# Kernel tuning notes

Hardware: AMD Instinct MI355X
Metric: run time of the kernel (lower is better)

The kernel has to match this reference:

```python
import jax, jax.numpy as jnp
import numpy as np

DIM = 1280
HEADS = 16
HD = DIM // HEADS  # 80
NSEG = 8
LSEG = 1024
SEQ = NSEG * LSEG  # 8192


def _rotate_half(x):
    x1, x2 = jnp.split(x, 2, axis=-1)
    return jnp.concatenate([-x2, x1], axis=-1)


def setup_inputs() -> dict:
    key = jax.random.key(0)
    ks = jax.random.split(key, 6)
    hidden_states = jax.random.normal(ks[0], (SEQ, DIM), dtype=jnp.float32)
    # rotary embedding table: per-position angles over head_dim
    inv_freq = 1.0 / (10000.0 ** (np.arange(0, HD, 2, dtype=np.float32) / HD))
    pos = np.arange(SEQ, dtype=np.float32)
    freqs = np.outer(pos, inv_freq)                    # [SEQ, HD/2]
    emb = np.concatenate([freqs, freqs], axis=-1)      # [SEQ, HD]
    cos = jnp.asarray(np.cos(emb), dtype=jnp.float32)
    sin = jnp.asarray(np.sin(emb), dtype=jnp.float32)
    w_scale = 1.0 / np.sqrt(DIM)
    qkv_w = jax.random.normal(ks[1], (DIM, 3 * DIM), dtype=jnp.float32) * w_scale
    qkv_b = jax.random.normal(ks[2], (3 * DIM,), dtype=jnp.float32) * 0.02
    proj_w = jax.random.normal(ks[3], (DIM, DIM), dtype=jnp.float32) * w_scale
    proj_b = jax.random.normal(ks[4], (DIM,), dtype=jnp.float32) * 0.02
    cu_seqlens = jnp.arange(NSEG + 1, dtype=jnp.int32) * LSEG
    return {
        "hidden_states": hidden_states,
        "cos": cos,
        "sin": sin,
        "qkv_w": qkv_w,
        "qkv_b": qkv_b,
        "proj_w": proj_w,
        "proj_b": proj_b,
        "cu_seqlens": cu_seqlens,
    }


def reference(hidden_states, cos, sin, qkv_w, qkv_b, proj_w, proj_b, cu_seqlens):
    S, D = hidden_states.shape
    n_seg = cu_seqlens.shape[0] - 1          # static
    L = S // n_seg                            # equal-length packed segments
    # fused QKV projection: [S, 3D] -> q, k, v each [S, H, hd]
    qkv = hidden_states @ qkv_w + qkv_b
    q, k, v = (t.reshape(S, HEADS, HD) for t in jnp.split(qkv, 3, axis=-1))
    # RoPE (computed in fp32, as in apply_rotary_pos_emb_vision)
    c = cos.astype(jnp.float32)[:, None, :]   # [S, 1, hd]
    s = sin.astype(jnp.float32)[:, None, :]
    qf = q.astype(jnp.float32)
    kf = k.astype(jnp.float32)
    q = (qf * c + _rotate_half(qf) * s).astype(q.dtype)
    k = (kf * c + _rotate_half(kf) * s).astype(k.dtype)
    # block-diagonal varlen attention == independent attention per segment
    qs = q.reshape(n_seg, L, HEADS, HD)
    ks = k.reshape(n_seg, L, HEADS, HD)
    vs = v.reshape(n_seg, L, HEADS, HD)
    scale = HD ** -0.5
    scores = jnp.einsum("nqhd,nkhd->nhqk", qs, ks) * scale
    probs = jax.nn.softmax(scores.astype(jnp.float32), axis=-1).astype(qs.dtype)
    out = jnp.einsum("nhqk,nkhd->nqhd", probs, vs)     # [n, L, H, hd]
    out = out.reshape(S, D)
    return out @ proj_w + proj_b
```

## Files before the change

### kernel.cpp

```cpp
#include <hip/hip_runtime.h>

#define SEQ   8192
#define DIM   1280
#define HEADS 16
#define HD    80
#define LSEG  1024
#define QKVD  3840

typedef unsigned short USHORT;
typedef __attribute__((ext_vector_type(8))) short bf16x8;
typedef __attribute__((ext_vector_type(4))) float f32x4;
typedef __attribute__((ext_vector_type(4))) USHORT u16x4;
typedef __attribute__((ext_vector_type(2))) unsigned uint2v;

#define CSF  0.16129832f
#define DTHR 71.554175f

__device__ __forceinline__ USHORT f2bf(float x) {
  unsigned u = __float_as_uint(x);
  u += 0x7fffu + ((u >> 16) & 1u);
  return (USHORT)(u >> 16);
}
__device__ __forceinline__ float bf2f(USHORT b) {
  return __uint_as_float(((unsigned)b) << 16);
}
__device__ __forceinline__ void gload16(const void* g, void* l) {
  __builtin_amdgcn_global_load_lds(
      (const __attribute__((address_space(1))) void*)g,
      (__attribute__((address_space(3))) void*)l, 16, 0, 0);
}
__device__ __forceinline__ unsigned cvtpk(float a, float b) {
  unsigned d;
  asm("v_cvt_pk_bf16_f32 %0, %1, %2" : "=v"(d) : "v"(a), "v"(b));
  return d;
}

__global__ __launch_bounds__(256) void conv_f2b(const float* __restrict__ in,
                                                USHORT* __restrict__ out, int n4) {
  int i = blockIdx.x * 256 + threadIdx.x;
  if (i >= n4) return;
  float4 v = reinterpret_cast<const float4*>(in)[i];
  USHORT* o = out + (size_t)i * 4;
  o[0] = f2bf(v.x); o[1] = f2bf(v.y); o[2] = f2bf(v.z); o[3] = f2bf(v.w);
}

__global__ __launch_bounds__(256) void conv_transpose(const float* __restrict__ W,
                                                      USHORT* __restrict__ Th,
                                                      int K, int N) {
  __shared__ float t[32][33];
  const int n0 = blockIdx.x * 32, k0 = blockIdx.y * 32;
  const int c = threadIdx.x & 31, r0 = threadIdx.x >> 5;
  for (int r = r0; r < 32; r += 8) t[r][c] = W[(size_t)(k0 + r) * N + n0 + c];
  __syncthreads();
  for (int r = r0; r < 32; r += 8)
    Th[(size_t)(n0 + r) * K + k0 + c] = f2bf(t[c][r]);
}

__global__ __launch_bounds__(256) void vtrans(const USHORT* __restrict__ qkv,
                                              USHORT* __restrict__ VtG) {
  __shared__ USHORT t[32][33];
  const int c0 = blockIdx.x * 32, s0 = blockIdx.y * 32;
  const int c = threadIdx.x & 31, r0 = threadIdx.x >> 5;
  for (int r = r0; r < 32; r += 8)
    t[r][c] = qkv[(size_t)(s0 + r) * QKVD + 2 * DIM + c0 + c];
  __syncthreads();
  for (int r = r0; r < 32; r += 8)
    VtG[(size_t)(c0 + r) * SEQ + s0 + c] = t[c][r];
}

__global__ __launch_bounds__(512, 2) void mfma_gemm256(
    const USHORT* __restrict__ Ah, const USHORT* __restrict__ Bh,
    const float* __restrict__ bias, USHORT* __restrict__ Cout,
    int M, int N, int K, int lda) {
  extern __shared__ USHORT sm[];

  const int tid = threadIdx.x;
  const int l = tid & 63;
  const int w = tid >> 6;
  const int fr = l & 15;
  const int g = l >> 4;
  const int nrow = M >> 8;
  const int nwg = nrow * (N >> 8);
  const int orig = blockIdx.x;
  const int wg = (orig & 7) * (nwg >> 3) + (orig >> 3);
  const int row0 = (wg % nrow) << 8;
  const int col0 = (wg / nrow) << 8;
  const int wr = (w >> 2) << 7;
  const int wc = (w & 3) << 6;

  const f32x4 fz = {0.f, 0.f, 0.f, 0.f};
  f32x4 acc[8][4];
#pragma unroll
  for (int m = 0; m < 8; ++m)
#pragma unroll
    for (int n = 0; n < 4; ++n) acc[m][n] = fz;

  const int NT = K >> 6;

  auto stage = [&](int t, int b) {
    const int k0 = t << 6;
#pragma unroll
    for (int i = 0; i < 4; ++i) {
      const int u = i * 512 + tid;
      const int row = u >> 3;
      const int c = (u & 7) ^ (row & 7);
      USHORT* dst = sm + (i * 512 + (w << 6)) * 8;
      gload16(Ah + (size_t)(row0 + row) * lda + k0 + c * 8,
              dst + b * 16384);
      gload16(Bh + (size_t)(col0 + row) * K + k0 + c * 8,
              dst + 32768 + b * 16384);
    }
  };

  stage(0, 0);
  stage(1, 1);

  for (int t = 0; t < NT; ++t) {
    const int cur = t & 1;
    asm volatile("s_waitcnt vmcnt(8)" ::: "memory");
    __builtin_amdgcn_sched_barrier(0);
    __builtin_amdgcn_s_barrier();
    __builtin_amdgcn_sched_barrier(0);
    bf16x8 ah[2][8], bh[2][4];
#pragma unroll
    for (int ks = 0; ks < 2; ++ks) {
      const int sl = (((ks << 2) + g) ^ (fr & 7)) << 3;
#pragma unroll
      for (int m = 0; m < 8; ++m)
        ah[ks][m] = *(const bf16x8*)
            &sm[cur * 16384 + (wr + m * 16 + fr) * 64 + sl];
#pragma unroll
      for (int n = 0; n < 4; ++n)
        bh[ks][n] = *(const bf16x8*)
            &sm[32768 + cur * 16384 + (wc + n * 16 + fr) * 64 + sl];
    }
    asm volatile("s_waitcnt lgkmcnt(0)" ::: "memory");
    __builtin_amdgcn_sched_barrier(0);
    __builtin_amdgcn_s_barrier();
    __builtin_amdgcn_sched_barrier(0);
    const int tn = (t + 2 < NT) ? t + 2 : t;
    stage(tn, cur);
    __builtin_amdgcn_sched_barrier(0);
    __builtin_amdgcn_s_setprio(1);
#pragma unroll
    for (int ks = 0; ks < 2; ++ks)
#pragma unroll
      for (int m = 0; m < 8; ++m)
#pragma unroll
        for (int n = 0; n < 4; ++n)
          acc[m][n] = __builtin_amdgcn_mfma_f32_16x16x32_bf16(
              ah[ks][m], bh[ks][n], acc[m][n], 0, 0, 0);
    __builtin_amdgcn_s_setprio(0);
  }

  asm volatile("s_waitcnt vmcnt(0)" ::: "memory");

  float bv[4];
#pragma unroll
  for (int n = 0; n < 4; ++n) bv[n] = bias[col0 + wc + n * 16 + fr];
#pragma unroll
  for (int m = 0; m < 8; ++m)
#pragma unroll
    for (int n = 0; n < 4; ++n)
#pragma unroll
      for (int r = 0; r < 4; ++r) {
        const float v = acc[m][n][r] + bv[n];
        const int row = row0 + wr + m * 16 + g * 4 + r;
        const int col = col0 + wc + n * 16 + fr;
        Cout[(size_t)row * N + col] = f2bf(v);
      }
}

template <int OUTBF>
__global__ __launch_bounds__(256) void mfma_gemm(
    const USHORT* __restrict__ Ah, const USHORT* __restrict__ Bh,
    const float* __restrict__ bias, void* __restrict__ Cout,
    int M, int N, int K, int lda) {
  __shared__ __align__(16) USHORT AhL[2][8192];
  __shared__ __align__(16) USHORT BhL[2][8192];

  const int tid = threadIdx.x;
  const int l = tid & 63;
  const int w = tid >> 6;
  const int nrow = M >> 7;
  const int nwg = nrow * (N >> 7);
  const int orig = blockIdx.x;
  const int wg = (orig & 7) * (nwg >> 3) + (orig >> 3);
  const int row0 = (wg % nrow) << 7;
  const int col0 = (wg / nrow) << 7;
  const int wr = (w >> 1) << 6;
  const int wc = (w & 1) << 6;

  const f32x4 fz = {0.f, 0.f, 0.f, 0.f};
  f32x4 acc[4][4];
#pragma unroll
  for (int m = 0; m < 4; ++m)
#pragma unroll
    for (int n = 0; n < 4; ++n) acc[m][n] = fz;

  const int fr = l & 15;
  const int g = l >> 4;

  const int NT = K >> 6;

  auto stage = [&](int t, int b) {
    const int k0 = t << 6;
#pragma unroll
    for (int i = 0; i < 4; ++i) {
      const int u = (w * 4 + i) * 64 + l;
      const int row = u >> 3;
      const int c = (u & 7) ^ (row & 7);
      gload16(Ah + (size_t)(row0 + row) * lda + k0 + c * 8,
              &AhL[b][(w * 4 + i) * 512]);
      gload16(Bh + (size_t)(col0 + row) * K + k0 + c * 8,
              &BhL[b][(w * 4 + i) * 512]);
    }
  };

  stage(0, 0);
  stage(1, 1);

  for (int t = 0; t < NT; ++t) {
    const int cur = t & 1;
    asm volatile("s_waitcnt vmcnt(8)" ::: "memory");
    __builtin_amdgcn_sched_barrier(0);
    __builtin_amdgcn_s_barrier();
    __builtin_amdgcn_sched_barrier(0);
    bf16x8 ah[2][4], bh[2][4];
#pragma unroll
    for (int ks = 0; ks < 2; ++ks)
#pragma unroll
      for (int m = 0; m < 4; ++m) {
        const int sl = (((ks << 2) + g) ^ (fr & 7)) << 3;
        ah[ks][m] = *(const bf16x8*)&AhL[cur][(wr + m * 16 + fr) * 64 + sl];
        bh[ks][m] = *(const bf16x8*)&BhL[cur][(wc + m * 16 + fr) * 64 + sl];
      }
    asm volatile("s_waitcnt lgkmcnt(0)" ::: "memory");
    __builtin_amdgcn_sched_barrier(0);
    __builtin_amdgcn_s_barrier();
    __builtin_amdgcn_sched_barrier(0);
    const int tn = (t + 2 < NT) ? t + 2 : t;
    stage(tn, cur);
    __builtin_amdgcn_sched_barrier(0);
    __builtin_amdgcn_s_setprio(1);
#pragma unroll
    for (int ks = 0; ks < 2; ++ks)
#pragma unroll
      for (int m = 0; m < 4; ++m)
#pragma unroll
        for (int n = 0; n < 4; ++n)
          acc[m][n] = __builtin_amdgcn_mfma_f32_16x16x32_bf16(
              ah[ks][m], bh[ks][n], acc[m][n], 0, 0, 0);
    __builtin_amdgcn_s_setprio(0);
  }

  asm volatile("s_waitcnt vmcnt(0)" ::: "memory");

  float bv[4];
#pragma unroll
  for (int n = 0; n < 4; ++n) bv[n] = bias[col0 + wc + n * 16 + fr];
#pragma unroll
  for (int m = 0; m < 4; ++m)
#pragma unroll
    for (int n = 0; n < 4; ++n)
#pragma unroll
      for (int r = 0; r < 4; ++r) {
        const float v = acc[m][n][r] + bv[n];
        const int row = row0 + wr + m * 16 + (l >> 4) * 4 + r;
        const int col = col0 + wc + n * 16 + fr;
        if (OUTBF)
          ((USHORT*)Cout)[(size_t)row * N + col] = f2bf(v);
        else
          ((float*)Cout)[(size_t)row * N + col] = v;
      }
}

__global__ __launch_bounds__(256) void rope_b(USHORT* __restrict__ qkv,
                                              const float* __restrict__ cosb,
                                              const float* __restrict__ sinb) {
  int idx = blockIdx.x * 256 + threadIdx.x;
  const int d4 = (idx % 10) * 4;
  int t = idx / 10;
  const int h = t % HEADS;
  t /= HEADS;
  const int qk = t & 1;
  const int s = t >> 1;
  USHORT* base = qkv + (size_t)s * QKVD + qk * DIM + h * HD;
  const u16x4 x1 = *(const u16x4*)&base[d4];
  const u16x4 x2 = *(const u16x4*)&base[d4 + 40];
  const f32x4 c1 = *(const f32x4*)&cosb[s * HD + d4];
  const f32x4 s1 = *(const f32x4*)&sinb[s * HD + d4];
  const f32x4 c2 = *(const f32x4*)&cosb[s * HD + d4 + 40];
  const f32x4 s2 = *(const f32x4*)&sinb[s * HD + d4 + 40];
  u16x4 o1, o2;
#pragma unroll
  for (int j = 0; j < 4; ++j) {
    const float a = bf2f(x1[j]), b = bf2f(x2[j]);
    o1[j] = f2bf(a * c1[j] - b * s1[j]);
    o2[j] = f2bf(b * c2[j] + a * s2[j]);
  }
  *(u16x4*)&base[d4] = o1;
  *(u16x4*)&base[d4 + 40] = o2;
}

__global__ void zero_ws(uint4* z) {
  z[threadIdx.x] = uint4{0u, 0u, 0u, 0u};
}

__global__ __launch_bounds__(256) void attn_mfma7(const USHORT* __restrict__ qkv,
                                                  const USHORT* __restrict__ VtG,
                                                  const USHORT* __restrict__ zbuf,
                                                  USHORT* __restrict__ aoB) {
  const int h = blockIdx.y;
  const int bx = blockIdx.x;
  const int qb = (bx & 7) * 8 + (bx >> 3);
  const int s0 = qb * 128;
  const int k0g = (s0 / LSEG) * LSEG;
  const int tid = threadIdx.x;
  const int w = tid >> 6, l = tid & 63;
  const int g = l >> 4, fr = l & 15;
  const int q0 = s0 + w * 32;

  __shared__ __align__(16) USHORT Kl[2][64 * 128];
  __shared__ __align__(16) USHORT Vl[2][96 * 64];
  __shared__ __align__(16) USHORT Pl[4][32 * 64];

  bf16x8 qb_frag[2][3];
#pragma unroll
  for (int nt2 = 0; nt2 < 2; ++nt2)
#pragma unroll
    for (int ks = 0; ks < 3; ++ks)
      qb_frag[nt2][ks] = *(const bf16x8*)
          &qkv[(size_t)(q0 + nt2 * 16 + fr) * QKVD + h * HD + ks * 32 + g * 8];

  const f32x4 fz = {0.f, 0.f, 0.f, 0.f};
  f32x4 oacc[2][5];
#pragma unroll
  for (int m = 0; m < 2; ++m)
#pragma unroll
    for (int n = 0; n < 5; ++n) oacc[m][n] = fz;
  float m_run[2] = {-3e38f, -3e38f};
  float l_run[2] = {0.f, 0.f};

  auto stageKV = [&](int kb, int b) {
    const size_t krow0 = (size_t)(k0g + kb * 64);
#pragma unroll
    for (int i = 0; i < 4; ++i) {
      const int t = (w * 4 + i) * 64 + l;
      const int row = t >> 4, c2 = t & 15, c = c2 ^ (row & 7);
      const USHORT* src =
          (c < 10) ? &qkv[(krow0 + row) * QKVD + DIM + h * HD + c * 8] : zbuf;
      gload16(src, &Kl[b][(w * 4 + i) * 512]);
    }
#pragma unroll
    for (int i = 0; i < 3; ++i) {
      const int u = (w * 3 + i) * 64 + l;
      const int row = u >> 3;
      const int c = (u & 7) ^ (row & 7);
      const USHORT* src = (row < 80)
          ? &VtG[(size_t)(h * HD + row) * SEQ + krow0 + c * 8] : zbuf;
      gload16(src, &Vl[b][(w * 3 + i) * 512]);
    }
  };

  stageKV(0, 0);
  stageKV(1, 1);

  for (int kb = 0; kb < 16; ++kb) {
    const int cur = kb & 1;
    asm volatile("s_waitcnt vmcnt(7)" ::: "memory");
    __builtin_amdgcn_sched_barrier(0);
    __builtin_amdgcn_s_barrier();
    __builtin_amdgcn_sched_barrier(0);

    f32x4 sc[4][2];
#pragma unroll
    for (int m = 0; m < 4; ++m)
#pragma unroll
      for (int nt2 = 0; nt2 < 2; ++nt2) sc[m][nt2] = fz;
#pragma unroll
    for (int ks = 0; ks < 3; ++ks)
#pragma unroll
      for (int m = 0; m < 4; ++m) {
        const bf16x8 kbf = *(const bf16x8*)
            &Kl[cur][(m * 16 + fr) * 128 + ((4 * ks + g) ^ (fr & 7)) * 8];
#pragma unroll
        for (int nt2 = 0; nt2 < 2; ++nt2)
          sc[m][nt2] = __builtin_amdgcn_mfma_f32_16x16x32_bf16(
              kbf, qb_frag[nt2][ks], sc[m][nt2], 0, 0, 0);
      }

    float rmax[2];
#pragma unroll
    for (int nt2 = 0; nt2 < 2; ++nt2) {
      float mx = -3e38f;
#pragma unroll
      for (int m = 0; m < 4; ++m)
#pragma unroll
        for (int j = 0; j < 4; ++j) mx = fmaxf(mx, sc[m][nt2][j]);
      mx = fmaxf(mx, __shfl_xor(mx, 16));
      mx = fmaxf(mx, __shfl_xor(mx, 32));
      rmax[nt2] = mx;
    }
    const bool need =
        (rmax[0] > m_run[0] + DTHR) || (rmax[1] > m_run[1] + DTHR);
    if (__any(need)) {
      float fac[2];
#pragma unroll
      for (int nt2 = 0; nt2 < 2; ++nt2) {
        const float mn = fmaxf(m_run[nt2], rmax[nt2]);
        fac[nt2] = exp2f((m_run[nt2] - mn) * CSF);
        m_run[nt2] = mn;
        l_run[nt2] *= fac[nt2];
      }
#pragma unroll
      for (int mt2 = 0; mt2 < 2; ++mt2)
#pragma unroll
        for (int j = 0; j < 4; ++j) {
          const float fb = __shfl(fac[mt2], 20 * g + j);
#pragma unroll
          for (int nt = 0; nt < 5; ++nt) oacc[mt2][nt][j] *= fb;
        }
    }
#pragma unroll
    for (int nt2 = 0; nt2 < 2; ++nt2) {
      const float mcs = m_run[nt2] * CSF;
      float ps = 0.f;
#pragma unroll
      for (int m = 0; m < 4; ++m) {
        float p[4];
#pragma unroll
        for (int j = 0; j < 4; ++j) {
          p[j] = exp2f(sc[m][nt2][j] * CSF - mcs);
          ps += p[j];
        }
        const uint2v pw = {cvtpk(p[0], p[1]), cvtpk(p[2], p[3])};
        const int chunk = 2 * m + (g >> 1);
        *(uint2v*)&Pl[w][(nt2 * 16 + fr) * 64 + ((chunk ^ (fr & 7)) << 3) +
                         ((g & 1) << 2)] = pw;
      }
      ps += __shfl_xor(ps, 16);
      ps += __shfl_xor(ps, 32);
      l_run[nt2] += ps;
    }

#pragma unroll
    for (int ks = 0; ks < 2; ++ks) {
      const int sl = (((ks << 2) + g) ^ (fr & 7)) << 3;
      bf16x8 pa[2];
#pragma unroll
      for (int mt2 = 0; mt2 < 2; ++mt2)
        pa[mt2] = *(const bf16x8*)&Pl[w][(mt2 * 16 + fr) * 64 + sl];
#pragma unroll
      for (int nt = 0; nt < 5; ++nt) {
        const bf16x8 vb = *(const bf16x8*)&Vl[cur][(nt * 16 + fr) * 64 + sl];
#pragma unroll
        for (int mt2 = 0; mt2 < 2; ++mt2)
          oacc[mt2][nt] = __builtin_amdgcn_mfma_f32_16x16x32_bf16(
              pa[mt2], vb, oacc[mt2][nt], 0, 0, 0);
      }
    }

    __builtin_amdgcn_s_barrier();
    __builtin_amdgcn_sched_barrier(0);
    const int kn = (kb + 2 < 16) ? kb + 2 : kb;
    stageKV(kn, cur);
    __builtin_amdgcn_sched_barrier(0);
  }

  asm volatile("s_waitcnt vmcnt(0)" ::: "memory");

  float linv[2][4];
#pragma unroll
  for (int mt2 = 0; mt2 < 2; ++mt2)
#pragma unroll
    for (int j = 0; j < 4; ++j)
      linv[mt2][j] = 1.f / __shfl(l_run[mt2], 20 * g + j);
#pragma unroll
  for (int mt2 = 0; mt2 < 2; ++mt2)
#pragma unroll
    for (int nt = 0; nt < 5; ++nt)
#pragma unroll
      for (int j = 0; j < 4; ++j) {
        const int row = s0 + w * 32 + mt2 * 16 + g * 4 + j;
        const int col = h * HD + nt * 16 + fr;
        aoB[(size_t)row * QKVD + col] = f2bf(oacc[mt2][nt][j] * linv[mt2][j]);
      }
}

extern "C" void kernel_launch(void* const* d_in, const int* in_sizes, int n_in,
                              void* d_out, int out_size, void* d_ws,
                              size_t ws_size, hipStream_t stream) {
  const float* hs = (const float*)d_in[0];
  const float* cosb = (const float*)d_in[1];
  const float* sinb = (const float*)d_in[2];
  const float* qkv_w = (const float*)d_in[3];
  const float* qkv_b = (const float*)d_in[4];
  const float* proj_w = (const float*)d_in[5];
  const float* proj_b = (const float*)d_in[6];
  char* ws = (char*)d_ws;

  USHORT* qkvB  = (USHORT*)(ws);
  USHORT* hsB   = (USHORT*)(ws + 62914560u);
  USHORT* qkvwT = (USHORT*)(ws + 83886080u);
  USHORT* pwT   = (USHORT*)(ws + 93716480u);
  USHORT* VtG   = hsB;
  USHORT* zbuf  = qkvwT;
  USHORT* aoB   = qkvB + 2 * DIM;

  hipFuncSetAttribute((const void*)mfma_gemm256,
                      hipFuncAttributeMaxDynamicSharedMemorySize, 131072);

  conv_f2b<<<SEQ * DIM / 4 / 256, 256, 0, stream>>>(hs, hsB, SEQ * DIM / 4);
  conv_transpose<<<dim3(QKVD / 32, DIM / 32), 256, 0, stream>>>(
      qkv_w, qkvwT, DIM, QKVD);
  conv_transpose<<<dim3(DIM / 32, DIM / 32), 256, 0, stream>>>(
      proj_w, pwT, DIM, DIM);

  mfma_gemm256<<<(SEQ / 256) * (QKVD / 256), 512, 131072, stream>>>(
      hsB, qkvwT, qkv_b, qkvB, SEQ, QKVD, DIM, DIM);
  rope_b<<<SEQ * HEADS * 2 * 10 / 256, 256, 0, stream>>>(qkvB, cosb, sinb);
  vtrans<<<dim3(DIM / 32, SEQ / 32), 256, 0, stream>>>(qkvB, VtG);
  zero_ws<<<1, 64, 0, stream>>>((uint4*)zbuf);
  attn_mfma7<<<dim3(SEQ / 128, HEADS), 256, 0, stream>>>(qkvB, VtG, zbuf, aoB);
  mfma_gemm<0><<<(SEQ / 128) * (DIM / 128), 256, 0, stream>>>(
      aoB, pwT, proj_b, d_out, SEQ, DIM, DIM, QKVD);
}
```

Measured before the change: 285.1 us.

## Keep attention P in registers via permuted V layout, trim LDS, add priorities

The V-transpose kernel now writes keys in a permuted column order. With that order, the bf16-packed probabilities from the QK^T MFMA output can be fed straight into the PV MFMA as the A operand. This removes the per-wave P round trip through LDS and the P shared buffer. The V LDS buffer shrinks from 96 to 80 rows, launch bounds ask for 3 blocks per CU, staging addresses are precomputed once, and s_setprio wraps the MFMA sections. The risks are the extra register pressure from the occupancy target and correctness depending on the permutation matching the MFMA fragment layout.

```diff
diff --git a/kernel.cpp b/kernel.cpp
--- a/kernel.cpp
+++ b/kernel.cpp
@@ -11,7 +11,7 @@
 typedef __attribute__((ext_vector_type(8))) short bf16x8;
 typedef __attribute__((ext_vector_type(4))) float f32x4;
 typedef __attribute__((ext_vector_type(4))) USHORT u16x4;
-typedef __attribute__((ext_vector_type(2))) unsigned uint2v;
+typedef __attribute__((ext_vector_type(4))) int i32x4;
 
 #define CSF  0.16129832f
 #define DTHR 71.554175f
@@ -64,8 +64,11 @@
   for (int r = r0; r < 32; r += 8)
     t[r][c] = qkv[(size_t)(s0 + r) * QKVD + 2 * DIM + c0 + c];
   __syncthreads();
+  const int pc = (s0 & 32) | c;
+  const int sc = (pc & 0x23) | ((pc & 0x10) >> 2) | ((pc & 0x0C) << 1);
+  const size_t col = (size_t)(s0 & ~63) + sc;
   for (int r = r0; r < 32; r += 8)
-    VtG[(size_t)(c0 + r) * SEQ + s0 + c] = t[c][r];
+    VtG[(size_t)(c0 + r) * SEQ + col] = t[c][r];
 }
 
 __global__ __launch_bounds__(512, 2) void mfma_gemm256(
@@ -307,10 +310,9 @@
   z[threadIdx.x] = uint4{0u, 0u, 0u, 0u};
 }
 
-__global__ __launch_bounds__(256) void attn_mfma7(const USHORT* __restrict__ qkv,
-                                                  const USHORT* __restrict__ VtG,
-                                                  const USHORT* __restrict__ zbuf,
-                                                  USHORT* __restrict__ aoB) {
+__global__ __launch_bounds__(256, 3) void attn_mfma8(
+    const USHORT* __restrict__ qkv, const USHORT* __restrict__ VtG,
+    const USHORT* __restrict__ zbuf, USHORT* __restrict__ aoB) {
   const int h = blockIdx.y;
   const int bx = blockIdx.x;
   const int qb = (bx & 7) * 8 + (bx >> 3);
@@ -322,8 +324,7 @@
   const int q0 = s0 + w * 32;
 
   __shared__ __align__(16) USHORT Kl[2][64 * 128];
-  __shared__ __align__(16) USHORT Vl[2][96 * 64];
-  __shared__ __align__(16) USHORT Pl[4][32 * 64];
+  __shared__ __align__(16) USHORT Vl[2][80 * 64];
 
   bf16x8 qb_frag[2][3];
 #pragma unroll
@@ -342,25 +343,39 @@
   float m_run[2] = {-3e38f, -3e38f};
   float l_run[2] = {0.f, 0.f};
 
+  const int nV = (w < 2) ? 3 : 2;
+  const int vbase = (w < 2) ? w * 3 : 6 + (w - 2) * 2;
+  const USHORT* ksrc[4];
+  int kstep[4];
+#pragma unroll
+  for (int i = 0; i < 4; ++i) {
+    const int t = (w * 4 + i) * 64 + l;
+    const int row = t >> 4, c = (t & 15) ^ (row & 7);
+    if (c < 10) {
+      ksrc[i] = qkv + (size_t)(k0g + row) * QKVD + DIM + h * HD + c * 8;
+      kstep[i] = 64 * QKVD;
+    } else {
+      ksrc[i] = zbuf;
+      kstep[i] = 0;
+    }
+  }
+  const USHORT* vsrc[3] = {zbuf, zbuf, zbuf};
+#pragma unroll
+  for (int i = 0; i < 3; ++i)
+    if (i < nV) {
+      const int u = (vbase + i) * 64 + l;
+      const int row = u >> 3, c = (u & 7) ^ (row & 7);
+      vsrc[i] = VtG + (size_t)(h * HD + row) * SEQ + k0g + c * 8;
+    }
+
   auto stageKV = [&](int kb, int b) {
-    const size_t krow0 = (size_t)(k0g + kb * 64);
-#pragma unroll
-    for (int i = 0; i < 4; ++i) {
-      const int t = (w * 4 + i) * 64 + l;
-      const int row = t >> 4, c2 = t & 15, c = c2 ^ (row & 7);
-      const USHORT* src =
-          (c < 10) ? &qkv[(krow0 + row) * QKVD + DIM + h * HD + c * 8] : zbuf;
-      gload16(src, &Kl[b][(w * 4 + i) * 512]);
-    }
-#pragma unroll
-    for (int i = 0; i < 3; ++i) {
-      const int u = (w * 3 + i) * 64 + l;
-      const int row = u >> 3;
-      const int c = (u & 7) ^ (row & 7);
-      const USHORT* src = (row < 80)
-          ? &VtG[(size_t)(h * HD + row) * SEQ + krow0 + c * 8] : zbuf;
-      gload16(src, &Vl[b][(w * 3 + i) * 512]);
-    }
+#pragma unroll
+    for (int i = 0; i < 4; ++i)
+      gload16(ksrc[i] + (size_t)kb * kstep[i], &Kl[b][(w * 4 + i) * 512]);
+#pragma unroll
+    for (int i = 0; i < 3; ++i)
+      if (i < nV)
+        gload16(vsrc[i] + kb * 64, &Vl[b][(vbase + i) * 512]);
   };
 
   stageKV(0, 0);
@@ -368,7 +383,11 @@
 
   for (int kb = 0; kb < 16; ++kb) {
     const int cur = kb & 1;
-    asm volatile("s_waitcnt vmcnt(7)" ::: "memory");
+    if (w < 2) {
+      asm volatile("s_waitcnt vmcnt(7)" ::: "memory");
+    } else {
+      asm volatile("s_waitcnt vmcnt(6)" ::: "memory");
+    }
     __builtin_amdgcn_sched_barrier(0);
     __builtin_amdgcn_s_barrier();
     __builtin_amdgcn_sched_barrier(0);
@@ -378,6 +397,7 @@
     for (int m = 0; m < 4; ++m)
 #pragma unroll
       for (int nt2 = 0; nt2 < 2; ++nt2) sc[m][nt2] = fz;
+    __builtin_amdgcn_s_setprio(1);
 #pragma unroll
     for (int ks = 0; ks < 3; ++ks)
 #pragma unroll
@@ -389,6 +409,7 @@
           sc[m][nt2] = __builtin_amdgcn_mfma_f32_16x16x32_bf16(
               kbf, qb_frag[nt2][ks], sc[m][nt2], 0, 0, 0);
       }
+    __builtin_amdgcn_s_setprio(0);
 
     float rmax[2];
 #pragma unroll
@@ -422,6 +443,7 @@
           for (int nt = 0; nt < 5; ++nt) oacc[mt2][nt][j] *= fb;
         }
     }
+    unsigned pkr[2][4][2];
 #pragma unroll
     for (int nt2 = 0; nt2 < 2; ++nt2) {
       const float mcs = m_run[nt2] * CSF;
@@ -434,10 +456,8 @@
           p[j] = exp2f(sc[m][nt2][j] * CSF - mcs);
           ps += p[j];
         }
-        const uint2v pw = {cvtpk(p[0], p[1]), cvtpk(p[2], p[3])};
-        const int chunk = 2 * m + (g >> 1);
-        *(uint2v*)&Pl[w][(nt2 * 16 + fr) * 64 + ((chunk ^ (fr & 7)) << 3) +
-                         ((g & 1) << 2)] = pw;
+        pkr[nt2][m][0] = cvtpk(p[0], p[1]);
+        pkr[nt2][m][1] = cvtpk(p[2], p[3]);
       }
       ps += __shfl_xor(ps, 16);
       ps += __shfl_xor(ps, 32);
@@ -447,18 +467,24 @@
 #pragma unroll
     for (int ks = 0; ks < 2; ++ks) {
       const int sl = (((ks << 2) + g) ^ (fr & 7)) << 3;
-      bf16x8 pa[2];
-#pragma unroll
-      for (int mt2 = 0; mt2 < 2; ++mt2)
-        pa[mt2] = *(const bf16x8*)&Pl[w][(mt2 * 16 + fr) * 64 + sl];
+      union { bf16x8 v8; i32x4 i4; } pa[2];
+#pragma unroll
+      for (int mt2 = 0; mt2 < 2; ++mt2) {
+        pa[mt2].i4[0] = (int)pkr[mt2][2 * ks][0];
+        pa[mt2].i4[1] = (int)pkr[mt2][2 * ks][1];
+        pa[mt2].i4[2] = (int)pkr[mt2][2 * ks + 1][0];
+        pa[mt2].i4[3] = (int)pkr[mt2][2 * ks + 1][1];
+      }
+      __builtin_amdgcn_s_setprio(1);
 #pragma unroll
       for (int nt = 0; nt < 5; ++nt) {
         const bf16x8 vb = *(const bf16x8*)&Vl[cur][(nt * 16 + fr) * 64 + sl];
 #pragma unroll
         for (int mt2 = 0; mt2 < 2; ++mt2)
           oacc[mt2][nt] = __builtin_amdgcn_mfma_f32_16x16x32_bf16(
-              pa[mt2], vb, oacc[mt2][nt], 0, 0, 0);
-      }
+              pa[mt2].v8, vb, oacc[mt2][nt], 0, 0, 0);
+      }
+      __builtin_amdgcn_s_setprio(0);
     }
 
     __builtin_amdgcn_s_barrier();
@@ -522,7 +548,7 @@
   rope_b<<<SEQ * HEADS * 2 * 10 / 256, 256, 0, stream>>>(qkvB, cosb, sinb);
   vtrans<<<dim3(DIM / 32, SEQ / 32), 256, 0, stream>>>(qkvB, VtG);
   zero_ws<<<1, 64, 0, stream>>>((uint4*)zbuf);
-  attn_mfma7<<<dim3(SEQ / 128, HEADS), 256, 0, stream>>>(qkvB, VtG, zbuf, aoB);
+  attn_mfma8<<<dim3(SEQ / 128, HEADS), 256, 0, stream>>>(qkvB, VtG, zbuf, aoB);
   mfma_gemm<0><<<(SEQ / 128) * (DIM / 128), 256, 0, stream>>>(
       aoB, pwT, proj_b, d_out, SEQ, DIM, DIM, QKVD);
 }
```

New measurement: 274.8 us. 1.04x faster.
